# Performance work log

Hardware: AMD Instinct MI355X
Metric: run time of the kernel (lower is better)

Reference implementation:

```python
import jax, jax.numpy as jnp
import numpy as np

H, W = 640, 640
C_IN, C_OUT = 3, 64
K, PAD = 7, 3          # 7x7 sparse conv, SAME padding (stride 1)
POOL_K, POOL_S = 3, 2  # valid 3x3 max pool, stride 2
N_SITES = 100000
BN_EPS = 1e-5


def setup_inputs() -> dict:
    key = jax.random.key(0)
    k1, k2, k3 = jax.random.split(key, 3)
    feature_map = jax.random.normal(k1, (H, W, C_IN), dtype=jnp.float32)
    update_location = jax.random.randint(k2, (N_SITES, 2), 0, min(H, W)).astype(jnp.int64)
    # kaiming-uniform-ish init for the 7x7x3 -> 64 conv weight
    fan_in = K * K * C_IN
    bound = np.sqrt(3.0 / fan_in).astype(np.float32)
    weight = jax.random.uniform(k3, (K, K, C_IN, C_OUT), jnp.float32, -bound, bound)
    return {
        "update_location": update_location,
        "feature_map": feature_map,
        "weight": weight,
        "gamma": jnp.ones((C_OUT,), jnp.float32),
        "beta": jnp.zeros((C_OUT,), jnp.float32),
        "running_mean": jnp.zeros((C_OUT,), jnp.float32),
        "running_var": jnp.ones((C_OUT,), jnp.float32),
    }


def reference(update_location, feature_map, weight, gamma, beta, running_mean, running_var):
    # ---- sparse (active-site) 7x7 conv: gather patches only at active sites ----
    fm = jnp.pad(feature_map, ((PAD, PAD), (PAD, PAD), (0, 0)))  # zero pad borders
    offs = jnp.arange(K)
    rows = update_location[:, 0, None] + offs          # [N, K] (pad offset = +PAD-PAD)
    cols = update_location[:, 1, None] + offs          # [N, K]
    patches = fm[rows[:, :, None], cols[:, None, :]]   # [N, K, K, C_IN]
    feats = jnp.einsum('nijc,ijco->no', patches, weight)  # [N, C_OUT]

    # ---- frozen BN + ReLU fused on active sites ----
    inv = gamma * jax.lax.rsqrt(running_var + BN_EPS)
    feats = jnp.maximum(feats * inv + (beta - running_mean * inv), 0.0)

    # ---- scatter active-site features into dense map (inactive sites stay 0) ----
    dense = jnp.zeros((H, W, C_OUT), feats.dtype).at[
        update_location[:, 0], update_location[:, 1]].set(feats)

    # ---- 3x3 stride-2 valid max pool (ReLU outputs >= 0, zeros elsewhere) ----
    pooled = jax.lax.reduce_window(
        dense, 0.0, jax.lax.max,
        (POOL_K, POOL_K, 1), (POOL_S, POOL_S, 1), 'VALID')  # [319, 319, C_OUT]
    return pooled
```

## Files before the change

kernel.cpp:

```cpp
#include <hip/hip_runtime.h>

#define HH 640
#define WW 640
#define COUT 64
#define KK 7
#define NS 100000
#define OHh 319
#define OWw 319
#define PWY 646
#define PWX 648
#define WGT_BLKS 7
#define OWNER_BLKS 391
#define PAD_BLKS 818
#define NBLK 1563
#define NWB (4 * KK * 64)

typedef _Float16 half2_t __attribute__((ext_vector_type(2)));
typedef _Float16 h8 __attribute__((ext_vector_type(8)));
typedef float f4 __attribute__((ext_vector_type(4)));
typedef uint4 u4a __attribute__((aligned(8)));

union H2U { unsigned u; half2_t h; };
union H8U { uint4 u; h8 h; _Float16 e[8]; };

__device__ __forceinline__ unsigned short f2bf(float x) {
    unsigned u = __float_as_uint(x);
    return (unsigned short)((u + 0x7FFFu + ((u >> 16) & 1u)) >> 16);
}
__device__ __forceinline__ float bf2f(unsigned short b) {
    return __uint_as_float((unsigned)b << 16);
}

__device__ __forceinline__ bool detect_is64(const int* __restrict__ loc) {
    const int smp = loc[1 + 2 * (int)(threadIdx.x & 63)];
    return __ballot(smp != 0) == 0ULL;
}

__global__ __launch_bounds__(256) void prep_kernel(
        const int* __restrict__ loc, const float* __restrict__ fm,
        const float* __restrict__ wgt, const float* __restrict__ gamma,
        const float* __restrict__ beta, const float* __restrict__ mean,
        const float* __restrict__ var,
        int* __restrict__ owner, uint2* __restrict__ pfm,
        uint4* __restrict__ wbg, float* __restrict__ bn,
        int* __restrict__ aidx) {
    if (blockIdx.x < WGT_BLKS) {
        const int e = blockIdx.x * 256 + threadIdx.x;
        const int t = e / (KK * 64);
        const int rem = e - t * KK * 64;
        const int i = rem >> 6, l = rem & 63;
        const int cout = t * 16 + (l & 15);
        const int q = l >> 4;
        H8U w;
        #pragma unroll
        for (int j = 0; j < 8; ++j) {
            const int kl = q * 8 + j, px = kl >> 2, ci = kl & 3;
            const float v = (px < KK && ci < 3)
                              ? wgt[((i * KK + px) * 3 + ci) * COUT + cout] : 0.0f;
            w.e[j] = (_Float16)v;
        }
        wbg[e] = w.u;
        if (blockIdx.x == 0 && threadIdx.x < COUT) {
            const int co = threadIdx.x;
            const float iv = gamma[co] * rsqrtf(var[co] + 1e-5f);
            bn[co] = iv;
            bn[COUT + co] = beta[co] - mean[co] * iv;
        }
    } else if (blockIdx.x < WGT_BLKS + OWNER_BLKS) {
        const bool is64 = detect_is64(loc);
        const int n = (blockIdx.x - WGT_BLKS) * 256 + threadIdx.x;
        if (n < NS) {
            int r, c;
            if (is64) { r = loc[4 * n]; c = loc[4 * n + 2]; }
            else      { r = loc[2 * n]; c = loc[2 * n + 1]; }
            atomicMax(&owner[r * WW + c], n);
            aidx[n] = r * PWX + c;
        }
    } else {
        const int pair = (blockIdx.x - WGT_BLKS - OWNER_BLKS) * 256 + threadIdx.x;
        const int pix = pair * 2;
        if (pix < PWY * PWX) {
            const int r = pix / PWX, c = pix - r * PWX;
            uint4 o;
            H2U a0, b0, a1, b1;
            a0.u = b0.u = a1.u = b1.u = 0;
            if (r >= 3 && r < 643) {
                const float* s = fm + ((size_t)(r - 3) * WW + (c - 3)) * 3;
                if (c >= 3 && c < 643) {
                    a0.h = half2_t{(_Float16)s[0], (_Float16)s[1]};
                    b0.h = half2_t{(_Float16)s[2], (_Float16)0};
                }
                if (c + 1 >= 3 && c + 1 < 643) {
                    a1.h = half2_t{(_Float16)s[3], (_Float16)s[4]};
                    b1.h = half2_t{(_Float16)s[5], (_Float16)0};
                }
            }
            o.x = a0.u; o.y = b0.u; o.z = a1.u; o.w = b1.u;
            *(uint4*)(pfm + pix) = o;
        }
    }
}

__global__ __launch_bounds__(256) void feats_kernel(
        const int* __restrict__ aidxg, const uint2* __restrict__ pfm,
        const uint4* __restrict__ wbg, const float* __restrict__ bn,
        unsigned short* __restrict__ feats) {
    __shared__ uint4 WB[NWB];
    const int lane = threadIdx.x & 63;
    const int wv = threadIdx.x >> 6;
    #pragma unroll
    for (int e = 0; e < NWB / 256; ++e)
        __builtin_amdgcn_global_load_lds(
            (const uint4*)(wbg + e * 256 + wv * 64 + lane),
            (uint4*)&WB[e * 256 + wv * 64], 16, 0, 0);
    __syncthreads();

    const int s = lane & 15;
    const int q = lane >> 4;
    const int n0 = (blockIdx.x * 4 + wv) * 16;
    if (n0 >= NS) return;

    const int nA = n0 + s;
    const int aidx = aidxg[nA] + 2 * q;

    H8U a[KK];
    #pragma unroll
    for (int i = 0; i < KK; ++i)
        a[i].u = *(const u4a*)(pfm + aidx + i * PWX);

    f4 acc[4] = {f4{0,0,0,0}, f4{0,0,0,0}, f4{0,0,0,0}, f4{0,0,0,0}};
    #pragma unroll
    for (int i = 0; i < KK; ++i) {
        #pragma unroll
        for (int t = 0; t < 4; ++t) {
            H8U b;
            b.u = WB[(t * KK + i) * 64 + lane];
            acc[t] = __builtin_amdgcn_mfma_f32_16x16x32_f16(b.h, a[i].h, acc[t], 0, 0, 0);
        }
    }

    unsigned short* dst = feats + (size_t)nA * COUT;
    #pragma unroll
    for (int t = 0; t < 4; ++t) {
        const float4 iv = *(const float4*)&bn[t * 16 + 4 * q];
        const float4 bi = *(const float4*)&bn[COUT + t * 16 + 4 * q];
        const unsigned short o0 = f2bf(fmaxf(acc[t][0] * iv.x + bi.x, 0.0f));
        const unsigned short o1 = f2bf(fmaxf(acc[t][1] * iv.y + bi.y, 0.0f));
        const unsigned short o2 = f2bf(fmaxf(acc[t][2] * iv.z + bi.z, 0.0f));
        const unsigned short o3 = f2bf(fmaxf(acc[t][3] * iv.w + bi.w, 0.0f));
        uint2 w;
        w.x = (unsigned)o0 | ((unsigned)o1 << 16);
        w.y = (unsigned)o2 | ((unsigned)o3 << 16);
        *(uint2*)(dst + t * 16 + 4 * q) = w;
    }
}

__global__ __launch_bounds__(256) void pool_kernel(
        const int* __restrict__ owner, const unsigned short* __restrict__ feats,
        float* __restrict__ out) {
    const int lane = threadIdx.x & 63;
    const int TPR = 80;
    const int task = __builtin_amdgcn_readfirstlane(blockIdx.x * 4 + (threadIdx.x >> 6));
    if (task >= OHh * TPR) return;
    const int oh = task / TPR, ow0 = (task % TPR) * 4;
    const int r0 = oh * 2, c0 = ow0 * 2;

    int ov[27];
    #pragma unroll
    for (int dy = 0; dy < 3; ++dy)
        #pragma unroll
        for (int dx = 0; dx < 9; ++dx)
            ov[dy * 9 + dx] =
                __builtin_amdgcn_readfirstlane(owner[(r0 + dy) * WW + c0 + dx]);

    float v[27];
    #pragma unroll
    for (int k = 0; k < 27; ++k) v[k] = 0.0f;
    #pragma unroll
    for (int k = 0; k < 27; ++k) {
        const int o = ov[k];
        if (o >= 0 && o < NS)
            v[k] = bf2f(feats[(size_t)o * COUT + lane]);
    }

    float colmax[9];
    #pragma unroll
    for (int x = 0; x < 9; ++x)
        colmax[x] = fmaxf(fmaxf(v[x], v[9 + x]), v[18 + x]);

    #pragma unroll
    for (int qq = 0; qq < 4; ++qq) {
        const int ow = ow0 + qq;
        if (ow >= OWw) break;
        const float m = fmaxf(fmaxf(colmax[2 * qq], colmax[2 * qq + 1]),
                              colmax[2 * qq + 2]);
        out[(size_t)(oh * OWw + ow) * COUT + lane] = m;
    }
}

extern "C" void kernel_launch(void* const* d_in, const int* in_sizes, int n_in,
                              void* d_out, int out_size, void* d_ws, size_t ws_size,
                              hipStream_t stream) {
    const int*   loc   = (const int*)d_in[0];
    const float* fm    = (const float*)d_in[1];
    const float* wgt   = (const float*)d_in[2];
    const float* gamma = (const float*)d_in[3];
    const float* beta  = (const float*)d_in[4];
    const float* mean  = (const float*)d_in[5];
    const float* var   = (const float*)d_in[6];
    float* out = (float*)d_out;

    char* ws = (char*)d_ws;
    int* owner = (int*)ws;
    uint2* pfm = (uint2*)(ws + 1638400);
    char* ws2 = ws + 1638400 + (size_t)PWY * PWX * 8;
    uint4* wbg = (uint4*)ws2;
    float* bn  = (float*)(ws2 + NWB * 16);
    int* aidx  = (int*)(ws2 + NWB * 16 + 512);
    unsigned short* feats =
        (unsigned short*)(ws2 + NWB * 16 + 512 + NS * 4);

    prep_kernel<<<WGT_BLKS + OWNER_BLKS + PAD_BLKS, 256, 0, stream>>>(
        loc, fm, wgt, gamma, beta, mean, var, owner, pfm, wbg, bn, aidx);
    feats_kernel<<<NBLK, 256, 0, stream>>>(aidx, pfm, wbg, bn, feats);
    pool_kernel<<<(OHh * 80 + 3) / 4, 256, 0, stream>>>(owner, feats, out);
}
```

Measured before the change: 114.2 us.

## Fuse padded fp16 feature map build and owner scatter into feats kernel

Removes the padded half-precision feature map pass and the separate owner/aidx pass from the prep kernel. The feats kernel now reads locations directly, does the owner atomicMax itself, and gathers fp32 input patches from the original feature map with bounds clamping, converting to fp16 in registers. This saves writing and reading a roughly 3.3MB padded buffer plus the aidx array, at the cost of more scattered, unaligned fp32 loads and bounds checks in the compute kernel. The owner atomics must still finish before the pool kernel, which the stream ordering provides.

```diff
diff --git a/kernel.cpp b/kernel.cpp
--- a/kernel.cpp
+++ b/kernel.cpp
@@ -7,20 +7,14 @@
 #define NS 100000
 #define OHh 319
 #define OWw 319
-#define PWY 646
-#define PWX 648
 #define WGT_BLKS 7
-#define OWNER_BLKS 391
-#define PAD_BLKS 818
 #define NBLK 1563
 #define NWB (4 * KK * 64)
 
 typedef _Float16 half2_t __attribute__((ext_vector_type(2)));
 typedef _Float16 h8 __attribute__((ext_vector_type(8)));
 typedef float f4 __attribute__((ext_vector_type(4)));
-typedef uint4 u4a __attribute__((aligned(8)));
-
-union H2U { unsigned u; half2_t h; };
+
 union H8U { uint4 u; h8 h; _Float16 e[8]; };
 
 __device__ __forceinline__ unsigned short f2bf(float x) {
@@ -37,74 +31,37 @@
 }
 
 __global__ __launch_bounds__(256) void prep_kernel(
-        const int* __restrict__ loc, const float* __restrict__ fm,
         const float* __restrict__ wgt, const float* __restrict__ gamma,
         const float* __restrict__ beta, const float* __restrict__ mean,
         const float* __restrict__ var,
-        int* __restrict__ owner, uint2* __restrict__ pfm,
-        uint4* __restrict__ wbg, float* __restrict__ bn,
-        int* __restrict__ aidx) {
-    if (blockIdx.x < WGT_BLKS) {
-        const int e = blockIdx.x * 256 + threadIdx.x;
-        const int t = e / (KK * 64);
-        const int rem = e - t * KK * 64;
-        const int i = rem >> 6, l = rem & 63;
-        const int cout = t * 16 + (l & 15);
-        const int q = l >> 4;
-        H8U w;
-        #pragma unroll
-        for (int j = 0; j < 8; ++j) {
-            const int kl = q * 8 + j, px = kl >> 2, ci = kl & 3;
-            const float v = (px < KK && ci < 3)
-                              ? wgt[((i * KK + px) * 3 + ci) * COUT + cout] : 0.0f;
-            w.e[j] = (_Float16)v;
-        }
-        wbg[e] = w.u;
-        if (blockIdx.x == 0 && threadIdx.x < COUT) {
-            const int co = threadIdx.x;
-            const float iv = gamma[co] * rsqrtf(var[co] + 1e-5f);
-            bn[co] = iv;
-            bn[COUT + co] = beta[co] - mean[co] * iv;
-        }
-    } else if (blockIdx.x < WGT_BLKS + OWNER_BLKS) {
-        const bool is64 = detect_is64(loc);
-        const int n = (blockIdx.x - WGT_BLKS) * 256 + threadIdx.x;
-        if (n < NS) {
-            int r, c;
-            if (is64) { r = loc[4 * n]; c = loc[4 * n + 2]; }
-            else      { r = loc[2 * n]; c = loc[2 * n + 1]; }
-            atomicMax(&owner[r * WW + c], n);
-            aidx[n] = r * PWX + c;
-        }
-    } else {
-        const int pair = (blockIdx.x - WGT_BLKS - OWNER_BLKS) * 256 + threadIdx.x;
-        const int pix = pair * 2;
-        if (pix < PWY * PWX) {
-            const int r = pix / PWX, c = pix - r * PWX;
-            uint4 o;
-            H2U a0, b0, a1, b1;
-            a0.u = b0.u = a1.u = b1.u = 0;
-            if (r >= 3 && r < 643) {
-                const float* s = fm + ((size_t)(r - 3) * WW + (c - 3)) * 3;
-                if (c >= 3 && c < 643) {
-                    a0.h = half2_t{(_Float16)s[0], (_Float16)s[1]};
-                    b0.h = half2_t{(_Float16)s[2], (_Float16)0};
-                }
-                if (c + 1 >= 3 && c + 1 < 643) {
-                    a1.h = half2_t{(_Float16)s[3], (_Float16)s[4]};
-                    b1.h = half2_t{(_Float16)s[5], (_Float16)0};
-                }
-            }
-            o.x = a0.u; o.y = b0.u; o.z = a1.u; o.w = b1.u;
-            *(uint4*)(pfm + pix) = o;
-        }
+        uint4* __restrict__ wbg, float* __restrict__ bn) {
+    const int e = blockIdx.x * 256 + threadIdx.x;
+    const int t = e / (KK * 64);
+    const int rem = e - t * KK * 64;
+    const int i = rem >> 6, l = rem & 63;
+    const int cout = t * 16 + (l & 15);
+    const int q = l >> 4;
+    H8U w;
+    #pragma unroll
+    for (int j = 0; j < 8; ++j) {
+        const int kl = q * 8 + j, px = kl >> 2, ci = kl & 3;
+        const float v = (px < KK && ci < 3)
+                          ? wgt[((i * KK + px) * 3 + ci) * COUT + cout] : 0.0f;
+        w.e[j] = (_Float16)v;
+    }
+    wbg[e] = w.u;
+    if (blockIdx.x == 0 && threadIdx.x < COUT) {
+        const int co = threadIdx.x;
+        const float iv = gamma[co] * rsqrtf(var[co] + 1e-5f);
+        bn[co] = iv;
+        bn[COUT + co] = beta[co] - mean[co] * iv;
     }
 }
 
 __global__ __launch_bounds__(256) void feats_kernel(
-        const int* __restrict__ aidxg, const uint2* __restrict__ pfm,
+        const int* __restrict__ loc, const float* __restrict__ fm,
         const uint4* __restrict__ wbg, const float* __restrict__ bn,
-        unsigned short* __restrict__ feats) {
+        int* __restrict__ owner, unsigned short* __restrict__ feats) {
     __shared__ uint4 WB[NWB];
     const int lane = threadIdx.x & 63;
     const int wv = threadIdx.x >> 6;
@@ -113,6 +70,7 @@
         __builtin_amdgcn_global_load_lds(
             (const uint4*)(wbg + e * 256 + wv * 64 + lane),
             (uint4*)&WB[e * 256 + wv * 64], 16, 0, 0);
+    const bool is64 = detect_is64(loc);
     __syncthreads();
 
     const int s = lane & 15;
@@ -121,12 +79,34 @@
     if (n0 >= NS) return;
 
     const int nA = n0 + s;
-    const int aidx = aidxg[nA] + 2 * q;
+    int rA, cA;
+    if (is64) { rA = loc[4 * nA]; cA = loc[4 * nA + 2]; }
+    else      { rA = loc[2 * nA]; cA = loc[2 * nA + 1]; }
+
+    if (q == 0) atomicMax(&owner[rA * WW + cA], nA);
 
     H8U a[KK];
     #pragma unroll
-    for (int i = 0; i < KK; ++i)
-        a[i].u = *(const u4a*)(pfm + aidx + i * PWX);
+    for (int i = 0; i < KK; ++i) {
+        const int rr = rA - 3 + i;
+        const int rrc = min(max(rr, 0), HH - 1);
+        const float* rowp = fm + (size_t)rrc * (WW * 3);
+        const bool rok = (rr >= 0) & (rr < HH);
+        #pragma unroll
+        for (int p = 0; p < 2; ++p) {
+            const int cc = cA - 3 + 2 * q + p;
+            const int ccc = min(max(cc, 0), WW - 1);
+            const bool ok = rok & (cc >= 0) & (cc < WW);
+            const float* pp = rowp + ccc * 3;
+            const float v0 = ok ? pp[0] : 0.0f;
+            const float v1 = ok ? pp[1] : 0.0f;
+            const float v2 = ok ? pp[2] : 0.0f;
+            a[i].e[p * 4 + 0] = (_Float16)v0;
+            a[i].e[p * 4 + 1] = (_Float16)v1;
+            a[i].e[p * 4 + 2] = (_Float16)v2;
+            a[i].e[p * 4 + 3] = (_Float16)0.0f;
+        }
+    }
 
     f4 acc[4] = {f4{0,0,0,0}, f4{0,0,0,0}, f4{0,0,0,0}, f4{0,0,0,0}};
     #pragma unroll
@@ -212,16 +192,13 @@
 
     char* ws = (char*)d_ws;
     int* owner = (int*)ws;
-    uint2* pfm = (uint2*)(ws + 1638400);
-    char* ws2 = ws + 1638400 + (size_t)PWY * PWX * 8;
+    char* ws2 = ws + 1638400;
     uint4* wbg = (uint4*)ws2;
     float* bn  = (float*)(ws2 + NWB * 16);
-    int* aidx  = (int*)(ws2 + NWB * 16 + 512);
     unsigned short* feats =
-        (unsigned short*)(ws2 + NWB * 16 + 512 + NS * 4);
-
-    prep_kernel<<<WGT_BLKS + OWNER_BLKS + PAD_BLKS, 256, 0, stream>>>(
-        loc, fm, wgt, gamma, beta, mean, var, owner, pfm, wbg, bn, aidx);
-    feats_kernel<<<NBLK, 256, 0, stream>>>(aidx, pfm, wbg, bn, feats);
+        (unsigned short*)(ws2 + NWB * 16 + 512);
+
+    prep_kernel<<<WGT_BLKS, 256, 0, stream>>>(wgt, gamma, beta, mean, var, wbg, bn);
+    feats_kernel<<<NBLK, 256, 0, stream>>>(loc, fm, wbg, bn, owner, feats);
     pool_kernel<<<(OHh * 80 + 3) / 4, 256, 0, stream>>>(owner, feats, out);
 }
```

Result: slower. 138.8 us (+21.5%).

## Fuse prep, conv and pool into one cooperative persistent kernel with grid syncs

Applied to the files above, without the earlier changes.

Merges the three kernels into one persistent cooperative kernel. Grid-stride loops cover each phase, and grid-wide barriers separate them, which removes two kernel launch gaps. The pool phase is also reworked: each wave now covers 8 outputs per strip, with lanes loading owner indices in parallel and broadcasting them via readlane. The catch is grid sync overhead and a grid size capped by occupancy, which may leave less parallelism in the memory-bound phases. Owner initialisation is assumed to happen outside this code, as before.

```diff
diff --git a/kernel.cpp b/kernel.cpp
--- a/kernel.cpp
+++ b/kernel.cpp
@@ -1,4 +1,7 @@
 #include <hip/hip_runtime.h>
+#include <hip/hip_cooperative_groups.h>
+
+namespace cg = cooperative_groups;
 
 #define HH 640
 #define WW 640
@@ -9,11 +12,11 @@
 #define OWw 319
 #define PWY 646
 #define PWX 648
-#define WGT_BLKS 7
-#define OWNER_BLKS 391
-#define PAD_BLKS 818
-#define NBLK 1563
 #define NWB (4 * KK * 64)
+#define NPAIR (PWY * PWX / 2)
+#define TPR 40
+#define TPB 256
+#define MAXGRID 1024
 
 typedef _Float16 half2_t __attribute__((ext_vector_type(2)));
 typedef _Float16 h8 __attribute__((ext_vector_type(8)));
@@ -36,16 +39,23 @@
     return __ballot(smp != 0) == 0ULL;
 }
 
-__global__ __launch_bounds__(256) void prep_kernel(
+__global__ __launch_bounds__(TPB, 4) void fused_kernel(
         const int* __restrict__ loc, const float* __restrict__ fm,
         const float* __restrict__ wgt, const float* __restrict__ gamma,
         const float* __restrict__ beta, const float* __restrict__ mean,
         const float* __restrict__ var,
         int* __restrict__ owner, uint2* __restrict__ pfm,
         uint4* __restrict__ wbg, float* __restrict__ bn,
-        int* __restrict__ aidx) {
-    if (blockIdx.x < WGT_BLKS) {
-        const int e = blockIdx.x * 256 + threadIdx.x;
+        int* __restrict__ aidx, unsigned short* __restrict__ feats,
+        float* __restrict__ out) {
+    __shared__ uint4 WB[NWB];
+    const int tid = threadIdx.x;
+    const int lane = tid & 63;
+    const int wv = tid >> 6;
+    const int gtid = blockIdx.x * TPB + tid;
+    const int gsz = gridDim.x * TPB;
+
+    for (int e = gtid; e < NWB; e += gsz) {
         const int t = e / (KK * 64);
         const int rem = e - t * KK * 64;
         const int i = rem >> 6, l = rem & 63;
@@ -60,56 +70,47 @@
             w.e[j] = (_Float16)v;
         }
         wbg[e] = w.u;
-        if (blockIdx.x == 0 && threadIdx.x < COUT) {
-            const int co = threadIdx.x;
-            const float iv = gamma[co] * rsqrtf(var[co] + 1e-5f);
-            bn[co] = iv;
-            bn[COUT + co] = beta[co] - mean[co] * iv;
-        }
-    } else if (blockIdx.x < WGT_BLKS + OWNER_BLKS) {
+    }
+    if (gtid < COUT) {
+        const float iv = gamma[gtid] * rsqrtf(var[gtid] + 1e-5f);
+        bn[gtid] = iv;
+        bn[COUT + gtid] = beta[gtid] - mean[gtid] * iv;
+    }
+    {
         const bool is64 = detect_is64(loc);
-        const int n = (blockIdx.x - WGT_BLKS) * 256 + threadIdx.x;
-        if (n < NS) {
+        for (int n = gtid; n < NS; n += gsz) {
             int r, c;
             if (is64) { r = loc[4 * n]; c = loc[4 * n + 2]; }
             else      { r = loc[2 * n]; c = loc[2 * n + 1]; }
             atomicMax(&owner[r * WW + c], n);
             aidx[n] = r * PWX + c;
         }
-    } else {
-        const int pair = (blockIdx.x - WGT_BLKS - OWNER_BLKS) * 256 + threadIdx.x;
+    }
+    for (int pair = gtid; pair < NPAIR; pair += gsz) {
         const int pix = pair * 2;
-        if (pix < PWY * PWX) {
-            const int r = pix / PWX, c = pix - r * PWX;
-            uint4 o;
-            H2U a0, b0, a1, b1;
-            a0.u = b0.u = a1.u = b1.u = 0;
-            if (r >= 3 && r < 643) {
-                const float* s = fm + ((size_t)(r - 3) * WW + (c - 3)) * 3;
-                if (c >= 3 && c < 643) {
-                    a0.h = half2_t{(_Float16)s[0], (_Float16)s[1]};
-                    b0.h = half2_t{(_Float16)s[2], (_Float16)0};
-                }
-                if (c + 1 >= 3 && c + 1 < 643) {
-                    a1.h = half2_t{(_Float16)s[3], (_Float16)s[4]};
-                    b1.h = half2_t{(_Float16)s[5], (_Float16)0};
-                }
-            }
-            o.x = a0.u; o.y = b0.u; o.z = a1.u; o.w = b1.u;
-            *(uint4*)(pfm + pix) = o;
-        }
-    }
-}
-
-__global__ __launch_bounds__(256) void feats_kernel(
-        const int* __restrict__ aidxg, const uint2* __restrict__ pfm,
-        const uint4* __restrict__ wbg, const float* __restrict__ bn,
-        unsigned short* __restrict__ feats) {
-    __shared__ uint4 WB[NWB];
-    const int lane = threadIdx.x & 63;
-    const int wv = threadIdx.x >> 6;
+        const int r = pix / PWX, c = pix - r * PWX;
+        uint4 o;
+        H2U a0, b0, a1, b1;
+        a0.u = b0.u = a1.u = b1.u = 0;
+        if (r >= 3 && r < 643) {
+            const float* s = fm + ((size_t)(r - 3) * WW + (c - 3)) * 3;
+            if (c >= 3 && c < 643) {
+                a0.h = half2_t{(_Float16)s[0], (_Float16)s[1]};
+                b0.h = half2_t{(_Float16)s[2], (_Float16)0};
+            }
+            if (c + 1 >= 3 && c + 1 < 643) {
+                a1.h = half2_t{(_Float16)s[3], (_Float16)s[4]};
+                b1.h = half2_t{(_Float16)s[5], (_Float16)0};
+            }
+        }
+        o.x = a0.u; o.y = b0.u; o.z = a1.u; o.w = b1.u;
+        *(uint4*)(pfm + pix) = o;
+    }
+
+    cg::this_grid().sync();
+
     #pragma unroll
-    for (int e = 0; e < NWB / 256; ++e)
+    for (int e = 0; e < NWB / TPB; ++e)
         __builtin_amdgcn_global_load_lds(
             (const uint4*)(wbg + e * 256 + wv * 64 + lane),
             (uint4*)&WB[e * 256 + wv * 64], 16, 0, 0);
@@ -117,84 +118,83 @@
 
     const int s = lane & 15;
     const int q = lane >> 4;
-    const int n0 = (blockIdx.x * 4 + wv) * 16;
-    if (n0 >= NS) return;
-
-    const int nA = n0 + s;
-    const int aidx = aidxg[nA] + 2 * q;
-
-    H8U a[KK];
-    #pragma unroll
-    for (int i = 0; i < KK; ++i)
-        a[i].u = *(const u4a*)(pfm + aidx + i * PWX);
-
-    f4 acc[4] = {f4{0,0,0,0}, f4{0,0,0,0}, f4{0,0,0,0}, f4{0,0,0,0}};
-    #pragma unroll
-    for (int i = 0; i < KK; ++i) {
+    const int gw = blockIdx.x * 4 + wv;
+    const int totw = gridDim.x * 4;
+
+    for (int wt = gw; wt < NS / 16; wt += totw) {
+        const int nA = wt * 16 + s;
+        const int ai = aidx[nA] + 2 * q;
+
+        H8U a[KK];
+        #pragma unroll
+        for (int i = 0; i < KK; ++i)
+            a[i].u = *(const u4a*)(pfm + ai + i * PWX);
+
+        f4 acc[4] = {f4{0,0,0,0}, f4{0,0,0,0}, f4{0,0,0,0}, f4{0,0,0,0}};
+        #pragma unroll
+        for (int i = 0; i < KK; ++i) {
+            #pragma unroll
+            for (int t = 0; t < 4; ++t) {
+                H8U b;
+                b.u = WB[(t * KK + i) * 64 + lane];
+                acc[t] = __builtin_amdgcn_mfma_f32_16x16x32_f16(b.h, a[i].h, acc[t], 0, 0, 0);
+            }
+        }
+
+        unsigned short* dst = feats + (size_t)nA * COUT;
         #pragma unroll
         for (int t = 0; t < 4; ++t) {
-            H8U b;
-            b.u = WB[(t * KK + i) * 64 + lane];
-            acc[t] = __builtin_amdgcn_mfma_f32_16x16x32_f16(b.h, a[i].h, acc[t], 0, 0, 0);
-        }
-    }
-
-    unsigned short* dst = feats + (size_t)nA * COUT;
-    #pragma unroll
-    for (int t = 0; t < 4; ++t) {
-        const float4 iv = *(const float4*)&bn[t * 16 + 4 * q];
-        const float4 bi = *(const float4*)&bn[COUT + t * 16 + 4 * q];
-        const unsigned short o0 = f2bf(fmaxf(acc[t][0] * iv.x + bi.x, 0.0f));
-        const unsigned short o1 = f2bf(fmaxf(acc[t][1] * iv.y + bi.y, 0.0f));
-        const unsigned short o2 = f2bf(fmaxf(acc[t][2] * iv.z + bi.z, 0.0f));
-        const unsigned short o3 = f2bf(fmaxf(acc[t][3] * iv.w + bi.w, 0.0f));
-        uint2 w;
-        w.x = (unsigned)o0 | ((unsigned)o1 << 16);
-        w.y = (unsigned)o2 | ((unsigned)o3 << 16);
-        *(uint2*)(dst + t * 16 + 4 * q) = w;
-    }
-}
-
-__global__ __launch_bounds__(256) void pool_kernel(
-        const int* __restrict__ owner, const unsigned short* __restrict__ feats,
-        float* __restrict__ out) {
-    const int lane = threadIdx.x & 63;
-    const int TPR = 80;
-    const int task = __builtin_amdgcn_readfirstlane(blockIdx.x * 4 + (threadIdx.x >> 6));
-    if (task >= OHh * TPR) return;
-    const int oh = task / TPR, ow0 = (task % TPR) * 4;
-    const int r0 = oh * 2, c0 = ow0 * 2;
-
-    int ov[27];
-    #pragma unroll
-    for (int dy = 0; dy < 3; ++dy)
-        #pragma unroll
-        for (int dx = 0; dx < 9; ++dx)
-            ov[dy * 9 + dx] =
-                __builtin_amdgcn_readfirstlane(owner[(r0 + dy) * WW + c0 + dx]);
-
-    float v[27];
-    #pragma unroll
-    for (int k = 0; k < 27; ++k) v[k] = 0.0f;
-    #pragma unroll
-    for (int k = 0; k < 27; ++k) {
-        const int o = ov[k];
-        if (o >= 0 && o < NS)
-            v[k] = bf2f(feats[(size_t)o * COUT + lane]);
-    }
-
-    float colmax[9];
-    #pragma unroll
-    for (int x = 0; x < 9; ++x)
-        colmax[x] = fmaxf(fmaxf(v[x], v[9 + x]), v[18 + x]);
-
-    #pragma unroll
-    for (int qq = 0; qq < 4; ++qq) {
-        const int ow = ow0 + qq;
-        if (ow >= OWw) break;
-        const float m = fmaxf(fmaxf(colmax[2 * qq], colmax[2 * qq + 1]),
-                              colmax[2 * qq + 2]);
-        out[(size_t)(oh * OWw + ow) * COUT + lane] = m;
+            const float4 iv = *(const float4*)&bn[t * 16 + 4 * q];
+            const float4 bi = *(const float4*)&bn[COUT + t * 16 + 4 * q];
+            const unsigned short o0 = f2bf(fmaxf(acc[t][0] * iv.x + bi.x, 0.0f));
+            const unsigned short o1 = f2bf(fmaxf(acc[t][1] * iv.y + bi.y, 0.0f));
+            const unsigned short o2 = f2bf(fmaxf(acc[t][2] * iv.z + bi.z, 0.0f));
+            const unsigned short o3 = f2bf(fmaxf(acc[t][3] * iv.w + bi.w, 0.0f));
+            uint2 w;
+            w.x = (unsigned)o0 | ((unsigned)o1 << 16);
+            w.y = (unsigned)o2 | ((unsigned)o3 << 16);
+            *(uint2*)(dst + t * 16 + 4 * q) = w;
+        }
+    }
+
+    cg::this_grid().sync();
+
+    const int dy3 = (lane >= 34) ? 2 : ((lane >= 17) ? 1 : 0);
+    const int dx3 = lane - dy3 * 17;
+
+    for (int strip = gw; strip < OHh * TPR; strip += totw) {
+        const int oh = strip / TPR, ow0 = (strip - oh * TPR) * 8;
+        const int r0 = oh * 2, c0 = ow0 * 2;
+
+        int o_l = -1;
+        if (lane < 51) o_l = owner[(r0 + dy3) * WW + c0 + dx3];
+
+        float colmax[17];
+        #pragma unroll
+        for (int j = 0; j < 17; ++j) colmax[j] = 0.0f;
+
+        #pragma unroll
+        for (int d = 0; d < 3; ++d) {
+            float v[17];
+            #pragma unroll
+            for (int j = 0; j < 17; ++j) {
+                const int o = __builtin_amdgcn_readlane(o_l, d * 17 + j);
+                v[j] = 0.0f;
+                if (o >= 0 && o < NS)
+                    v[j] = bf2f(feats[(size_t)o * COUT + lane]);
+            }
+            #pragma unroll
+            for (int j = 0; j < 17; ++j) colmax[j] = fmaxf(colmax[j], v[j]);
+        }
+
+        #pragma unroll
+        for (int w = 0; w < 8; ++w) {
+            const int ow = ow0 + w;
+            if (ow >= OWw) break;
+            const float m = fmaxf(fmaxf(colmax[2 * w], colmax[2 * w + 1]),
+                                  colmax[2 * w + 2]);
+            out[(size_t)(oh * OWw + ow) * COUT + lane] = m;
+        }
     }
 }
 
@@ -220,8 +220,23 @@
     unsigned short* feats =
         (unsigned short*)(ws2 + NWB * 16 + 512 + NS * 4);
 
-    prep_kernel<<<WGT_BLKS + OWNER_BLKS + PAD_BLKS, 256, 0, stream>>>(
-        loc, fm, wgt, gamma, beta, mean, var, owner, pfm, wbg, bn, aidx);
-    feats_kernel<<<NBLK, 256, 0, stream>>>(aidx, pfm, wbg, bn, feats);
-    pool_kernel<<<(OHh * 80 + 3) / 4, 256, 0, stream>>>(owner, feats, out);
-}
+    static int grid = 0;
+    if (grid == 0) {
+        int mb = 0;
+        hipOccupancyMaxActiveBlocksPerMultiprocessor(&mb, (const void*)fused_kernel,
+                                                     TPB, 0);
+        hipDeviceProp_t prop;
+        hipGetDeviceProperties(&prop, 0);
+        int g = mb * prop.multiProcessorCount;
+        if (g < 256) g = 256;
+        if (g > MAXGRID) g = MAXGRID;
+        grid = g;
+    }
+
+    void* args[] = {(void*)&loc, (void*)&fm, (void*)&wgt, (void*)&gamma,
+                    (void*)&beta, (void*)&mean, (void*)&var, (void*)&owner,
+                    (void*)&pfm, (void*)&wbg, (void*)&bn, (void*)&aidx,
+                    (void*)&feats, (void*)&out};
+    hipLaunchCooperativeKernel((const void*)fused_kernel, dim3(grid), dim3(TPB),
+                               args, 0, stream);
+}
```

Result: slower. 287.1 us (+151.4%).
